# Kernel optimization log

Measured on AMD Instinct MI355X. Metric: run time of the kernel, lower is better.

The kernel has to match this reference:

```python
import jax, jax.numpy as jnp
import numpy as np

N = 8192
IN_DIM = 256
OUT_DIM = 256
NEG_INF = -9e15


def setup_inputs() -> dict:
    key = jax.random.key(0)
    k1, k2, k3, k4, k5 = jax.random.split(key, 5)
    worker_x = jax.random.normal(k1, (N, IN_DIM), dtype=jnp.float32)
    ww_adj = jax.random.randint(k2, (N, N), 0, 2, dtype=jnp.int32)
    # learned params (xavier-ish scales)
    W = jax.random.normal(k3, (IN_DIM, OUT_DIM), dtype=jnp.float32) * (1.0 / np.sqrt(IN_DIM))
    a_src = jax.random.normal(k4, (OUT_DIM, 1), dtype=jnp.float32) * (1.414 / np.sqrt(OUT_DIM))
    a_dst = jax.random.normal(k5, (OUT_DIM, 1), dtype=jnp.float32) * (1.414 / np.sqrt(OUT_DIM))
    return {"worker_x": worker_x, "ww_adj": ww_adj, "W": W, "a_src": a_src, "a_dst": a_dst}


def reference(worker_x, ww_adj, W, a_src, a_dst):
    Wh = worker_x @ W                       # [N, out_dim]
    f_src = Wh @ a_src                      # [N, 1]
    f_dst = Wh @ a_dst                      # [N, 1]
    e = jax.nn.leaky_relu(f_src + f_dst.T, negative_slope=0.2)  # [N, N]
    attention = jnp.where(ww_adj > 0, e, NEG_INF)
    attention = jax.nn.softmax(attention, axis=-1)
    h_prime = attention @ Wh                # [N, out_dim]
    return jax.nn.elu(h_prime)
```

## Files before the change

kernel.cpp:

```cpp
#include <hip/hip_runtime.h>
#include <stdint.h>

typedef __attribute__((ext_vector_type(8))) short short8;
typedef __attribute__((ext_vector_type(4))) float f32x4;
typedef __attribute__((ext_vector_type(4))) _Float16 h16x4;

#define LOG2E 1.4426950408889634f

#define OFF_WTT   0u
#define OFF_WHTB  131072u
#define OFF_FSRC  12713984u
#define OFF_FDST  12746752u
#define OFF_MKEY  12779520u
#define OFF_LP    12779584u
#define OFF_ACCH  13041728u

__device__ __forceinline__ unsigned short f2bf(float f) {
    union { float f; unsigned int i; } v; v.f = f;
    unsigned int u = v.i;
    return (unsigned short)((u + 0x7FFFu + ((u >> 16) & 1u)) >> 16);
}

__global__ void k0_init(const float* __restrict__ W,
                        unsigned short* __restrict__ WTt,
                        unsigned int* __restrict__ Mkey) {
    int idx = blockIdx.x * 256 + threadIdx.x;
    int i = idx >> 8, o = idx & 255;
    WTt[(i >> 5) * 8192 + ((i >> 3) & 3) * 2048 + o * 8 + (i & 7)] = f2bf(W[idx]);
    if (idx == 0) *Mkey = 0u;
}

__global__ __launch_bounds__(256, 2)
void k1_stage1(const float* __restrict__ X,
               const unsigned short* __restrict__ WTt,
               const float* __restrict__ a_src,
               const float* __restrict__ a_dst,
               unsigned short* __restrict__ WhTb,
               float* __restrict__ f_src,
               float* __restrict__ f_dst,
               unsigned int* __restrict__ Mkey) {
    __shared__ __align__(16) unsigned short Bt[8192];
    __shared__ float fsum[64];
    const int t = threadIdx.x, w = t >> 6, lane = t & 63, l15 = lane & 15, q = lane >> 4;
    const int rg = w & 1, cg = w >> 1;
    const int i0 = blockIdx.x * 32;
    const int arow = i0 + rg * 16 + l15;

    if (t < 64) fsum[t] = 0.f;

    float as[8], ad[8];
#pragma unroll
    for (int ci = 0; ci < 8; ++ci) {
        int col = cg * 128 + ci * 16 + l15;
        as[ci] = a_src[col]; ad[ci] = a_dst[col];
    }

    f32x4 acc[8];
#pragma unroll
    for (int ci = 0; ci < 8; ++ci) acc[ci] = (f32x4)0.f;

    for (int ks = 0; ks < 8; ++ks) {
        __syncthreads();
        {
            const uint4* src = (const uint4*)(WTt + ks * 8192);
            uint4* dst = (uint4*)Bt;
            dst[t] = src[t]; dst[256 + t] = src[256 + t];
            dst[512 + t] = src[512 + t]; dst[768 + t] = src[768 + t];
        }
        __syncthreads();
        const float* xp = X + (size_t)arow * 256 + ks * 32 + q * 8;
        float4 xa = *(const float4*)xp;
        float4 xb = *(const float4*)(xp + 4);
        short8 a;
        a[0] = (short)f2bf(xa.x); a[1] = (short)f2bf(xa.y);
        a[2] = (short)f2bf(xa.z); a[3] = (short)f2bf(xa.w);
        a[4] = (short)f2bf(xb.x); a[5] = (short)f2bf(xb.y);
        a[6] = (short)f2bf(xb.z); a[7] = (short)f2bf(xb.w);
#pragma unroll
        for (int ci = 0; ci < 8; ++ci) {
            short8 b = *(const short8*)((const char*)Bt + q * 4096 + (cg * 128 + ci * 16 + l15) * 16);
            acc[ci] = __builtin_amdgcn_mfma_f32_16x16x32_bf16(a, b, acc[ci], 0, 0, 0);
        }
    }

#pragma unroll
    for (int ci = 0; ci < 8; ++ci) {
        int col = cg * 128 + ci * 16 + l15;
        ushort4 v;
        v.x = f2bf(acc[ci][0]); v.y = f2bf(acc[ci][1]);
        v.z = f2bf(acc[ci][2]); v.w = f2bf(acc[ci][3]);
        size_t flat = (size_t)(i0 >> 5) * 8192 + (size_t)(rg * 2 + (q >> 1)) * 2048
                      + (size_t)col * 8 + (q & 1) * 4;
        *(ushort4*)(WhTb + flat) = v;
    }

#pragma unroll
    for (int reg = 0; reg < 4; ++reg) {
        float ps = 0.f, pd = 0.f;
#pragma unroll
        for (int ci = 0; ci < 8; ++ci) {
            ps += acc[ci][reg] * as[ci];
            pd += acc[ci][reg] * ad[ci];
        }
#pragma unroll
        for (int m = 1; m < 16; m <<= 1) {
            ps += __shfl_xor(ps, m, 64);
            pd += __shfl_xor(pd, m, 64);
        }
        if (l15 == 0) {
            atomicAdd(&fsum[rg * 16 + q * 4 + reg], ps);
            atomicAdd(&fsum[32 + rg * 16 + q * 4 + reg], pd);
        }
    }
    __syncthreads();
    if (t < 32) {
        int row = i0 + t;
        float ps = fsum[t], pd = fsum[32 + t];
        f_src[row] = ps;
        f_dst[row] = pd;
        union { float f; unsigned int u; } cv; cv.f = pd;
        unsigned int key = (cv.u & 0x80000000u) ? ~cv.u : (cv.u | 0x80000000u);
        atomicMax(Mkey, key);
    }
}

__global__ __launch_bounds__(256, 2)
void k2_fused(const int* __restrict__ adj,
              const unsigned short* __restrict__ WhTb,
              const float* __restrict__ f_src,
              const float* __restrict__ f_dst,
              const unsigned int* __restrict__ Mkey,
              float* __restrict__ Lp,
              _Float16* __restrict__ ACCh) {
    const int t = threadIdx.x, w = t >> 6, lane = t & 63, l15 = lane & 15, q = lane >> 4;
    const int i0 = blockIdx.x * 128;
    const int jc = blockIdx.y;
    const int jb0 = jc * 1024;
    const int jw0 = jc * 32;

    unsigned int key = *Mkey;
    union { unsigned int u; float f; } mv;
    mv.u = (key & 0x80000000u) ? (key & 0x7FFFFFFFu) : ~key;
    const float Mf = mv.f;
    const int rA = i0 + w * 32 + l15;
    const float fsA = f_src[rA], fsB = f_src[rA + 16];
    float vA = fsA + Mf; const float mcA = fmaxf(vA, 0.2f * vA) * LOG2E;
    float vB = fsB + Mf; const float mcB = fmaxf(vB, 0.2f * vB) * LOG2E;

    const int* adjA = adj + (size_t)rA * 8192 + jb0 + q * 8;
    const int* adjB = adj + (size_t)(rA + 16) * 8192 + jb0 + q * 8;
    const float* fdp = f_dst + jb0 + q * 8;
    const unsigned short* Bbase = WhTb + (size_t)jw0 * 8192 + q * 2048 + l15 * 8;

    f32x4 accA[16], accB[16];
#pragma unroll
    for (int ci = 0; ci < 16; ++ci) { accA[ci] = (f32x4)0.f; accB[ci] = (f32x4)0.f; }
    float lsA = 0.f, lsB = 0.f;

    int4 pA0 = *(const int4*)(adjA);
    int4 pA1 = *(const int4*)(adjA + 4);
    int4 pB0 = *(const int4*)(adjB);
    int4 pB1 = *(const int4*)(adjB + 4);
    float4 pf0 = *(const float4*)(fdp);
    float4 pf1 = *(const float4*)(fdp + 4);

    for (int js = 0; js < 32; ++js) {
        float fdv[8] = { pf0.x, pf0.y, pf0.z, pf0.w, pf1.x, pf1.y, pf1.z, pf1.w };
        int aAv[8] = { pA0.x, pA0.y, pA0.z, pA0.w, pA1.x, pA1.y, pA1.z, pA1.w };
        int aBv[8] = { pB0.x, pB0.y, pB0.z, pB0.w, pB1.x, pB1.y, pB1.z, pB1.w };

        short8 fragA, fragB;
#pragma unroll
        for (int k = 0; k < 8; ++k) {
            float tA = fsA + fdv[k];
            float eA = fmaxf(tA, 0.2f * tA);
            float pA = __builtin_amdgcn_exp2f(__builtin_fmaf(eA, LOG2E, -mcA));
            pA = (aAv[k] > 0) ? pA : 0.f;
            lsA += pA; fragA[k] = (short)f2bf(pA);
            float tB = fsB + fdv[k];
            float eB = fmaxf(tB, 0.2f * tB);
            float pB = __builtin_amdgcn_exp2f(__builtin_fmaf(eB, LOG2E, -mcB));
            pB = (aBv[k] > 0) ? pB : 0.f;
            lsB += pB; fragB[k] = (short)f2bf(pB);
        }

        int jn = (js + 1) & 31;
        pA0 = *(const int4*)(adjA + jn * 32);
        pA1 = *(const int4*)(adjA + jn * 32 + 4);
        pB0 = *(const int4*)(adjB + jn * 32);
        pB1 = *(const int4*)(adjB + jn * 32 + 4);
        pf0 = *(const float4*)(fdp + jn * 32);
        pf1 = *(const float4*)(fdp + jn * 32 + 4);

        const unsigned short* bp = Bbase + (size_t)js * 8192;
        short8 bf[8];
#pragma unroll
        for (int ci = 0; ci < 8; ++ci) bf[ci] = *(const short8*)(bp + ci * 128);
#pragma unroll
        for (int ci = 0; ci < 8; ++ci) {
            accA[ci] = __builtin_amdgcn_mfma_f32_16x16x32_bf16(fragA, bf[ci], accA[ci], 0, 0, 0);
            accB[ci] = __builtin_amdgcn_mfma_f32_16x16x32_bf16(fragB, bf[ci], accB[ci], 0, 0, 0);
        }
#pragma unroll
        for (int ci = 0; ci < 8; ++ci) bf[ci] = *(const short8*)(bp + (ci + 8) * 128);
#pragma unroll
        for (int ci = 0; ci < 8; ++ci) {
            accA[8 + ci] = __builtin_amdgcn_mfma_f32_16x16x32_bf16(fragA, bf[ci], accA[8 + ci], 0, 0, 0);
            accB[8 + ci] = __builtin_amdgcn_mfma_f32_16x16x32_bf16(fragB, bf[ci], accB[8 + ci], 0, 0, 0);
        }
    }

    lsA += __shfl_xor(lsA, 16, 64); lsA += __shfl_xor(lsA, 32, 64);
    lsB += __shfl_xor(lsB, 16, 64); lsB += __shfl_xor(lsB, 32, 64);
    if (lane < 16) {
        Lp[(size_t)jc * 8192 + i0 + w * 32 + lane] = lsA;
        Lp[(size_t)jc * 8192 + i0 + w * 32 + 16 + lane] = lsB;
    }

    _Float16* ap = ACCh + (size_t)jc * 2097152;
#pragma unroll
    for (int ci = 0; ci < 16; ++ci) {
#pragma unroll
        for (int reg = 0; reg < 4; ++reg) {
            int rowA = i0 + w * 32 + q * 4 + reg;
            ap[(size_t)rowA * 256 + ci * 16 + l15] = (_Float16)accA[ci][reg];
            ap[(size_t)(rowA + 16) * 256 + ci * 16 + l15] = (_Float16)accB[ci][reg];
        }
    }
}

__global__ void k4_final(const _Float16* __restrict__ ACCh,
                         const float* __restrict__ Lp,
                         float* __restrict__ out) {
    int gid = blockIdx.x * 256 + threadIdx.x;
    int i = gid >> 6;
    float s0 = 0.f, s1 = 0.f, s2 = 0.f, s3 = 0.f;
#pragma unroll
    for (int jc = 0; jc < 8; ++jc) {
        h16x4 v = *(const h16x4*)(ACCh + (size_t)jc * 2097152 + (size_t)gid * 4);
        s0 += (float)v[0]; s1 += (float)v[1]; s2 += (float)v[2]; s3 += (float)v[3];
    }
    float L = 0.f;
#pragma unroll
    for (int jc = 0; jc < 8; ++jc) L += Lp[jc * 8192 + i];
    float inv = (L > 0.f) ? (1.0f / L) : 0.f;
    float h0 = s0 * inv, h1 = s1 * inv, h2 = s2 * inv, h3 = s3 * inv;
    float4 o;
    o.x = (h0 > 0.f) ? h0 : expm1f(h0);
    o.y = (h1 > 0.f) ? h1 : expm1f(h1);
    o.z = (h2 > 0.f) ? h2 : expm1f(h2);
    o.w = (h3 > 0.f) ? h3 : expm1f(h3);
    *(float4*)(out + (size_t)gid * 4) = o;
}

extern "C" void kernel_launch(void* const* d_in, const int* in_sizes, int n_in,
                              void* d_out, int out_size, void* d_ws, size_t ws_size,
                              hipStream_t stream) {
    (void)in_sizes; (void)n_in; (void)out_size; (void)ws_size;
    const float* X   = (const float*)d_in[0];
    const int*   adj = (const int*)d_in[1];
    const float* W   = (const float*)d_in[2];
    const float* a_s = (const float*)d_in[3];
    const float* a_d = (const float*)d_in[4];

    char* ws = (char*)d_ws;
    unsigned short* WTt  = (unsigned short*)(ws + OFF_WTT);
    unsigned short* WhTb = (unsigned short*)(ws + OFF_WHTB);
    float*          fsrc = (float*)(ws + OFF_FSRC);
    float*          fdst = (float*)(ws + OFF_FDST);
    unsigned int*   Mkey = (unsigned int*)(ws + OFF_MKEY);
    float*          Lp   = (float*)(ws + OFF_LP);
    _Float16*       ACCh = (_Float16*)(ws + OFF_ACCH);
    float*          out  = (float*)d_out;

    k0_init<<<dim3(256), dim3(256), 0, stream>>>(W, WTt, Mkey);
    k1_stage1<<<dim3(256), dim3(256), 0, stream>>>(X, WTt, a_s, a_d, WhTb, fsrc, fdst, Mkey);
    k2_fused<<<dim3(64, 8), dim3(256), 0, stream>>>(adj, WhTb, fsrc, fdst, Mkey, Lp, ACCh);
    k4_final<<<dim3(2048), dim3(256), 0, stream>>>(ACCh, Lp, out);
}
```

Measured before the change: 469.3 us.

## Stage WhT tiles into LDS with double-buffered global_load_lds prefetch

Each block now cooperatively copies the WhT tile for the next j-step into a double-buffered LDS region using direct global-to-LDS loads. The per-wave B fragments are then read from LDS rather than each wave fetching them separately from global memory, and f_dst for the block's column chunk is cached once in shared memory. The aim is to cut redundant global/L2 traffic across the four waves and overlap the next tile's load with the current MFMAs. In exchange it adds a __syncthreads per iteration and about 33KB of LDS, which may lower occupancy at 2 blocks per CU.

```diff
diff --git a/kernel.cpp b/kernel.cpp
--- a/kernel.cpp
+++ b/kernel.cpp
@@ -19,6 +19,13 @@
     union { float f; unsigned int i; } v; v.f = f;
     unsigned int u = v.i;
     return (unsigned short)((u + 0x7FFFu + ((u >> 16) & 1u)) >> 16);
+}
+
+__device__ __forceinline__ void stage16(const unsigned short* g, unsigned short* l) {
+    __builtin_amdgcn_global_load_lds(
+        (const __attribute__((address_space(1))) unsigned int*)g,
+        (__attribute__((address_space(3))) unsigned int*)l,
+        16, 0, 0);
 }
 
 __global__ void k0_init(const float* __restrict__ W,
@@ -132,6 +139,8 @@
               const unsigned int* __restrict__ Mkey,
               float* __restrict__ Lp,
               _Float16* __restrict__ ACCh) {
+    __shared__ __align__(16) unsigned short Bt[2][8192];
+    __shared__ float fd_s[1024];
     const int t = threadIdx.x, w = t >> 6, lane = t & 63, l15 = lane & 15, q = lane >> 4;
     const int i0 = blockIdx.x * 128;
     const int jc = blockIdx.y;
@@ -147,10 +156,16 @@
     float vA = fsA + Mf; const float mcA = fmaxf(vA, 0.2f * vA) * LOG2E;
     float vB = fsB + Mf; const float mcB = fmaxf(vB, 0.2f * vB) * LOG2E;
 
+    { float4* d = (float4*)fd_s; d[t] = ((const float4*)(f_dst + jb0))[t]; }
+    {
+        const unsigned short* gsrc = WhTb + (size_t)jw0 * 8192;
+#pragma unroll
+        for (int s = 0; s < 4; ++s)
+            stage16(gsrc + s * 2048 + t * 8, &Bt[0][s * 2048 + w * 512]);
+    }
+
     const int* adjA = adj + (size_t)rA * 8192 + jb0 + q * 8;
     const int* adjB = adj + (size_t)(rA + 16) * 8192 + jb0 + q * 8;
-    const float* fdp = f_dst + jb0 + q * 8;
-    const unsigned short* Bbase = WhTb + (size_t)jw0 * 8192 + q * 2048 + l15 * 8;
 
     f32x4 accA[16], accB[16];
 #pragma unroll
@@ -161,14 +176,24 @@
     int4 pA1 = *(const int4*)(adjA + 4);
     int4 pB0 = *(const int4*)(adjB);
     int4 pB1 = *(const int4*)(adjB + 4);
-    float4 pf0 = *(const float4*)(fdp);
-    float4 pf1 = *(const float4*)(fdp + 4);
+    __syncthreads();
 
     for (int js = 0; js < 32; ++js) {
-        float fdv[8] = { pf0.x, pf0.y, pf0.z, pf0.w, pf1.x, pf1.y, pf1.z, pf1.w };
+        const int buf = js & 1;
+        const int jn = (js + 1) & 31;
+
+        {
+            const unsigned short* gsrc = WhTb + (size_t)(jw0 + jn) * 8192;
+#pragma unroll
+            for (int s = 0; s < 4; ++s)
+                stage16(gsrc + s * 2048 + t * 8, &Bt[buf ^ 1][s * 2048 + w * 512]);
+        }
+
+        const float* fdp = fd_s + js * 32 + q * 8;
+        float4 f0 = *(const float4*)fdp, f1 = *(const float4*)(fdp + 4);
+        float fdv[8] = { f0.x, f0.y, f0.z, f0.w, f1.x, f1.y, f1.z, f1.w };
         int aAv[8] = { pA0.x, pA0.y, pA0.z, pA0.w, pA1.x, pA1.y, pA1.z, pA1.w };
         int aBv[8] = { pB0.x, pB0.y, pB0.z, pB0.w, pB1.x, pB1.y, pB1.z, pB1.w };
-
         short8 fragA, fragB;
 #pragma unroll
         for (int k = 0; k < 8; ++k) {
@@ -184,30 +209,20 @@
             lsB += pB; fragB[k] = (short)f2bf(pB);
         }
 
-        int jn = (js + 1) & 31;
         pA0 = *(const int4*)(adjA + jn * 32);
         pA1 = *(const int4*)(adjA + jn * 32 + 4);
         pB0 = *(const int4*)(adjB + jn * 32);
         pB1 = *(const int4*)(adjB + jn * 32 + 4);
-        pf0 = *(const float4*)(fdp + jn * 32);
-        pf1 = *(const float4*)(fdp + jn * 32 + 4);
-
-        const unsigned short* bp = Bbase + (size_t)js * 8192;
-        short8 bf[8];
-#pragma unroll
-        for (int ci = 0; ci < 8; ++ci) bf[ci] = *(const short8*)(bp + ci * 128);
-#pragma unroll
-        for (int ci = 0; ci < 8; ++ci) {
-            accA[ci] = __builtin_amdgcn_mfma_f32_16x16x32_bf16(fragA, bf[ci], accA[ci], 0, 0, 0);
-            accB[ci] = __builtin_amdgcn_mfma_f32_16x16x32_bf16(fragB, bf[ci], accB[ci], 0, 0, 0);
-        }
-#pragma unroll
-        for (int ci = 0; ci < 8; ++ci) bf[ci] = *(const short8*)(bp + (ci + 8) * 128);
-#pragma unroll
-        for (int ci = 0; ci < 8; ++ci) {
-            accA[8 + ci] = __builtin_amdgcn_mfma_f32_16x16x32_bf16(fragA, bf[ci], accA[8 + ci], 0, 0, 0);
-            accB[8 + ci] = __builtin_amdgcn_mfma_f32_16x16x32_bf16(fragB, bf[ci], accB[8 + ci], 0, 0, 0);
-        }
+
+        const char* base = (const char*)&Bt[buf][0] + q * 4096 + l15 * 16;
+#pragma unroll
+        for (int ci = 0; ci < 16; ++ci) {
+            short8 bf = *(const short8*)(base + ci * 256);
+            accA[ci] = __builtin_amdgcn_mfma_f32_16x16x32_bf16(fragA, bf, accA[ci], 0, 0, 0);
+            accB[ci] = __builtin_amdgcn_mfma_f32_16x16x32_bf16(fragB, bf, accB[ci], 0, 0, 0);
+        }
+
+        __syncthreads();
     }
 
     lsA += __shfl_xor(lsA, 16, 64); lsA += __shfl_xor(lsA, 32, 64);
```

After: 444.3 us. 5.3% less time.

## Halve rows per wave and double-buffer WhT fragments in registers

Applied to the files above, without the earlier changes.

Each wave now handles 16 rows instead of 32, so the grid doubles to 1024 blocks, and the per-wave accumulator count halves. The freed registers hold two full sets of B fragments, which are prefetched one step ahead, along with adjacency and f_dst loads for two steps. The goal is to hide global-load latency behind the MFMAs and raise occupancy. In exchange, each B fragment is reused by only one row-tile instead of two, which doubles global and L2 traffic for WhT.

```diff
diff --git a/kernel.cpp b/kernel.cpp
--- a/kernel.cpp
+++ b/kernel.cpp
@@ -133,7 +133,7 @@
               float* __restrict__ Lp,
               _Float16* __restrict__ ACCh) {
     const int t = threadIdx.x, w = t >> 6, lane = t & 63, l15 = lane & 15, q = lane >> 4;
-    const int i0 = blockIdx.x * 128;
+    const int i0 = blockIdx.x * 64;
     const int jc = blockIdx.y;
     const int jb0 = jc * 1024;
     const int jw0 = jc * 32;
@@ -142,89 +142,98 @@
     union { unsigned int u; float f; } mv;
     mv.u = (key & 0x80000000u) ? (key & 0x7FFFFFFFu) : ~key;
     const float Mf = mv.f;
-    const int rA = i0 + w * 32 + l15;
-    const float fsA = f_src[rA], fsB = f_src[rA + 16];
+    const int rA = i0 + w * 16 + l15;
+    const float fsA = f_src[rA];
     float vA = fsA + Mf; const float mcA = fmaxf(vA, 0.2f * vA) * LOG2E;
-    float vB = fsB + Mf; const float mcB = fmaxf(vB, 0.2f * vB) * LOG2E;
 
     const int* adjA = adj + (size_t)rA * 8192 + jb0 + q * 8;
-    const int* adjB = adj + (size_t)(rA + 16) * 8192 + jb0 + q * 8;
     const float* fdp = f_dst + jb0 + q * 8;
     const unsigned short* Bbase = WhTb + (size_t)jw0 * 8192 + q * 2048 + l15 * 8;
 
-    f32x4 accA[16], accB[16];
-#pragma unroll
-    for (int ci = 0; ci < 16; ++ci) { accA[ci] = (f32x4)0.f; accB[ci] = (f32x4)0.f; }
-    float lsA = 0.f, lsB = 0.f;
-
-    int4 pA0 = *(const int4*)(adjA);
-    int4 pA1 = *(const int4*)(adjA + 4);
-    int4 pB0 = *(const int4*)(adjB);
-    int4 pB1 = *(const int4*)(adjB + 4);
-    float4 pf0 = *(const float4*)(fdp);
-    float4 pf1 = *(const float4*)(fdp + 4);
-
-    for (int js = 0; js < 32; ++js) {
-        float fdv[8] = { pf0.x, pf0.y, pf0.z, pf0.w, pf1.x, pf1.y, pf1.z, pf1.w };
-        int aAv[8] = { pA0.x, pA0.y, pA0.z, pA0.w, pA1.x, pA1.y, pA1.z, pA1.w };
-        int aBv[8] = { pB0.x, pB0.y, pB0.z, pB0.w, pB1.x, pB1.y, pB1.z, pB1.w };
-
-        short8 fragA, fragB;
-#pragma unroll
-        for (int k = 0; k < 8; ++k) {
-            float tA = fsA + fdv[k];
-            float eA = fmaxf(tA, 0.2f * tA);
-            float pA = __builtin_amdgcn_exp2f(__builtin_fmaf(eA, LOG2E, -mcA));
-            pA = (aAv[k] > 0) ? pA : 0.f;
-            lsA += pA; fragA[k] = (short)f2bf(pA);
-            float tB = fsB + fdv[k];
-            float eB = fmaxf(tB, 0.2f * tB);
-            float pB = __builtin_amdgcn_exp2f(__builtin_fmaf(eB, LOG2E, -mcB));
-            pB = (aBv[k] > 0) ? pB : 0.f;
-            lsB += pB; fragB[k] = (short)f2bf(pB);
-        }
-
-        int jn = (js + 1) & 31;
-        pA0 = *(const int4*)(adjA + jn * 32);
-        pA1 = *(const int4*)(adjA + jn * 32 + 4);
-        pB0 = *(const int4*)(adjB + jn * 32);
-        pB1 = *(const int4*)(adjB + jn * 32 + 4);
-        pf0 = *(const float4*)(fdp + jn * 32);
-        pf1 = *(const float4*)(fdp + jn * 32 + 4);
-
-        const unsigned short* bp = Bbase + (size_t)js * 8192;
-        short8 bf[8];
-#pragma unroll
-        for (int ci = 0; ci < 8; ++ci) bf[ci] = *(const short8*)(bp + ci * 128);
-#pragma unroll
-        for (int ci = 0; ci < 8; ++ci) {
-            accA[ci] = __builtin_amdgcn_mfma_f32_16x16x32_bf16(fragA, bf[ci], accA[ci], 0, 0, 0);
-            accB[ci] = __builtin_amdgcn_mfma_f32_16x16x32_bf16(fragB, bf[ci], accB[ci], 0, 0, 0);
-        }
-#pragma unroll
-        for (int ci = 0; ci < 8; ++ci) bf[ci] = *(const short8*)(bp + (ci + 8) * 128);
-#pragma unroll
-        for (int ci = 0; ci < 8; ++ci) {
-            accA[8 + ci] = __builtin_amdgcn_mfma_f32_16x16x32_bf16(fragA, bf[ci], accA[8 + ci], 0, 0, 0);
-            accB[8 + ci] = __builtin_amdgcn_mfma_f32_16x16x32_bf16(fragB, bf[ci], accB[8 + ci], 0, 0, 0);
+    f32x4 acc[16];
+#pragma unroll
+    for (int ci = 0; ci < 16; ++ci) acc[ci] = (f32x4)0.f;
+    float lsA = 0.f;
+
+    short8 bf0[16], bf1[16];
+#pragma unroll
+    for (int ci = 0; ci < 16; ++ci) bf0[ci] = *(const short8*)(Bbase + ci * 128);
+    int4  a0_0 = *(const int4*)(adjA),        a0_1 = *(const int4*)(adjA + 4);
+    float4 f0_0 = *(const float4*)(fdp),      f0_1 = *(const float4*)(fdp + 4);
+    int4  a1_0 = *(const int4*)(adjA + 32),   a1_1 = *(const int4*)(adjA + 36);
+    float4 f1_0 = *(const float4*)(fdp + 32), f1_1 = *(const float4*)(fdp + 36);
+
+#pragma unroll 1
+    for (int js2 = 0; js2 < 16; ++js2) {
+        const int js = js2 * 2;
+        {
+            const int jn = (js + 1) & 31;
+            const unsigned short* bp = Bbase + (size_t)jn * 8192;
+#pragma unroll
+            for (int ci = 0; ci < 16; ++ci) bf1[ci] = *(const short8*)(bp + ci * 128);
+
+            float fdv[8] = { f0_0.x, f0_0.y, f0_0.z, f0_0.w, f0_1.x, f0_1.y, f0_1.z, f0_1.w };
+            int   aAv[8] = { a0_0.x, a0_0.y, a0_0.z, a0_0.w, a0_1.x, a0_1.y, a0_1.z, a0_1.w };
+            short8 fragA;
+#pragma unroll
+            for (int k = 0; k < 8; ++k) {
+                float tA = fsA + fdv[k];
+                float eA = fmaxf(tA, 0.2f * tA);
+                float pA = __builtin_amdgcn_exp2f(__builtin_fmaf(eA, LOG2E, -mcA));
+                pA = (aAv[k] > 0) ? pA : 0.f;
+                lsA += pA; fragA[k] = (short)f2bf(pA);
+            }
+
+            const int jp = (js + 2) & 31;
+            a0_0 = *(const int4*)(adjA + jp * 32);
+            a0_1 = *(const int4*)(adjA + jp * 32 + 4);
+            f0_0 = *(const float4*)(fdp + jp * 32);
+            f0_1 = *(const float4*)(fdp + jp * 32 + 4);
+
+#pragma unroll
+            for (int ci = 0; ci < 16; ++ci)
+                acc[ci] = __builtin_amdgcn_mfma_f32_16x16x32_bf16(fragA, bf0[ci], acc[ci], 0, 0, 0);
+        }
+        {
+            const int jn = (js + 2) & 31;
+            const unsigned short* bp = Bbase + (size_t)jn * 8192;
+#pragma unroll
+            for (int ci = 0; ci < 16; ++ci) bf0[ci] = *(const short8*)(bp + ci * 128);
+
+            float fdv[8] = { f1_0.x, f1_0.y, f1_0.z, f1_0.w, f1_1.x, f1_1.y, f1_1.z, f1_1.w };
+            int   aAv[8] = { a1_0.x, a1_0.y, a1_0.z, a1_0.w, a1_1.x, a1_1.y, a1_1.z, a1_1.w };
+            short8 fragA;
+#pragma unroll
+            for (int k = 0; k < 8; ++k) {
+                float tA = fsA + fdv[k];
+                float eA = fmaxf(tA, 0.2f * tA);
+                float pA = __builtin_amdgcn_exp2f(__builtin_fmaf(eA, LOG2E, -mcA));
+                pA = (aAv[k] > 0) ? pA : 0.f;
+                lsA += pA; fragA[k] = (short)f2bf(pA);
+            }
+
+            const int jp = (js + 3) & 31;
+            a1_0 = *(const int4*)(adjA + jp * 32);
+            a1_1 = *(const int4*)(adjA + jp * 32 + 4);
+            f1_0 = *(const float4*)(fdp + jp * 32);
+            f1_1 = *(const float4*)(fdp + jp * 32 + 4);
+
+#pragma unroll
+            for (int ci = 0; ci < 16; ++ci)
+                acc[ci] = __builtin_amdgcn_mfma_f32_16x16x32_bf16(fragA, bf1[ci], acc[ci], 0, 0, 0);
         }
     }
 
     lsA += __shfl_xor(lsA, 16, 64); lsA += __shfl_xor(lsA, 32, 64);
-    lsB += __shfl_xor(lsB, 16, 64); lsB += __shfl_xor(lsB, 32, 64);
-    if (lane < 16) {
-        Lp[(size_t)jc * 8192 + i0 + w * 32 + lane] = lsA;
-        Lp[(size_t)jc * 8192 + i0 + w * 32 + 16 + lane] = lsB;
-    }
+    if (lane < 16) Lp[(size_t)jc * 8192 + i0 + w * 16 + lane] = lsA;
 
     _Float16* ap = ACCh + (size_t)jc * 2097152;
 #pragma unroll
     for (int ci = 0; ci < 16; ++ci) {
 #pragma unroll
         for (int reg = 0; reg < 4; ++reg) {
-            int rowA = i0 + w * 32 + q * 4 + reg;
-            ap[(size_t)rowA * 256 + ci * 16 + l15] = (_Float16)accA[ci][reg];
-            ap[(size_t)(rowA + 16) * 256 + ci * 16 + l15] = (_Float16)accB[ci][reg];
+            int row = i0 + w * 16 + q * 4 + reg;
+            ap[(size_t)row * 256 + ci * 16 + l15] = (_Float16)acc[ci][reg];
         }
     }
 }
@@ -275,6 +284,6 @@
 
     k0_init<<<dim3(256), dim3(256), 0, stream>>>(W, WTt, Mkey);
     k1_stage1<<<dim3(256), dim3(256), 0, stream>>>(X, WTt, a_s, a_d, WhTb, fsrc, fdst, Mkey);
-    k2_fused<<<dim3(64, 8), dim3(256), 0, stream>>>(adj, WhTb, fsrc, fdst, Mkey, Lp, ACCh);
+    k2_fused<<<dim3(128, 8), dim3(256), 0, stream>>>(adj, WhTb, fsrc, fdst, Mkey, Lp, ACCh);
     k4_final<<<dim3(2048), dim3(256), 0, stream>>>(ACCh, Lp, out);
 }
```

New measurement: 548.1 us. 1.17x slower.
